# Kernel tuning notes

Measured on AMD Instinct MI355X. Metric: run time of the kernel, lower is better.

The kernel has to match this reference:

```python
import jax, jax.numpy as jnp
import numpy as np

D_MODEL = 1024
NHEAD = 16
EPS = 1e-5


def layer_norm(x, scale, bias):
    mu = jnp.mean(x, axis=-1, keepdims=True)
    var = jnp.var(x, axis=-1, keepdims=True)
    return (x - mu) * jax.lax.rsqrt(var + EPS) * scale + bias


def setup_inputs() -> dict:
    key = jax.random.key(0)
    ks = jax.random.split(key, 8)
    B, S, D = 4, 2048, D_MODEL
    s = 1.0 / np.sqrt(D)
    return {
        "x": jax.random.normal(ks[0], (B, S, D), dtype=jnp.float32),
        "Wq": jax.random.normal(ks[1], (D, D), dtype=jnp.float32) * s,
        "Wk": jax.random.normal(ks[2], (D, D), dtype=jnp.float32) * s,
        "Wv": jax.random.normal(ks[3], (D, D), dtype=jnp.float32) * s,
        "W1": jax.random.normal(ks[4], (D, D), dtype=jnp.float32) * s,
        "b1": jnp.zeros((D,), dtype=jnp.float32),
        "W2": jax.random.normal(ks[5], (D, D), dtype=jnp.float32) * s,
        "b2": jnp.zeros((D,), dtype=jnp.float32),
        "ln1_scale": jnp.ones((D,), dtype=jnp.float32),
        "ln1_bias": jnp.zeros((D,), dtype=jnp.float32),
        "ln2_scale": jnp.ones((D,), dtype=jnp.float32),
        "ln2_bias": jnp.zeros((D,), dtype=jnp.float32),
    }


def reference(x, Wq, Wk, Wv, W1, b1, W2, b2, ln1_scale, ln1_bias, ln2_scale, ln2_bias):
    B, S, D = x.shape
    H = NHEAD
    dh = D // H
    x = layer_norm(x, ln1_scale, ln1_bias)
    # torch Linear: y = x @ W.T (no bias for q/k/v)
    q = jnp.einsum('bsd,ed->bse', x, Wq).reshape(B, S, H, dh).transpose(0, 2, 1, 3)
    k = jnp.einsum('bsd,ed->bse', x, Wk).reshape(B, S, H, dh).transpose(0, 2, 1, 3)
    v = jnp.einsum('bsd,ed->bse', x, Wv).reshape(B, S, H, dh).transpose(0, 2, 1, 3)
    # NOTE: original module applies NO 1/sqrt(dh) scaling — kept faithful.
    scores = jnp.einsum('bhqd,bhkd->bhqk', q, k)
    attn = jax.nn.softmax(scores, axis=-1)  # dropout is identity in eval
    att = jnp.einsum('bhqk,bhkd->bhqd', attn, v)
    att = att.transpose(0, 2, 1, 3).reshape(B, S, D)
    xt = layer_norm(x + att, ln2_scale, ln2_bias)
    h = jax.nn.relu(jnp.einsum('bsd,ed->bse', xt, W1) + b1)
    ffn = jnp.einsum('bsd,ed->bse', h, W2) + b2
    return xt + ffn
```

## Files before the change

kernel.cpp:

```cpp
#include <hip/hip_runtime.h>
#include <stdint.h>

typedef unsigned short u16;
typedef __attribute__((ext_vector_type(4))) float f32x4;
typedef _Float16 h16;
typedef __attribute__((ext_vector_type(8))) _Float16 f16x8;
typedef __attribute__((ext_vector_type(4))) _Float16 h16x4;
typedef __attribute__((ext_vector_type(2))) __fp16 fp16v2;

#define DMODEL 1024
#define SEQ    2048
#define BATCH  4
#define NHEAD  16
#define DH     64
#define NTOK   (BATCH*SEQ)
#define BH     (BATCH*NHEAD)
#define EPS    1e-5f
#define LOG2E  1.44269504f

__device__ __forceinline__ void gload_lds16(const void* g, void* l){
  __builtin_amdgcn_global_load_lds((__attribute__((address_space(1))) unsigned int*)g,
                                   (__attribute__((address_space(3))) unsigned int*)l,
                                   16, 0, 0);
}

__device__ __forceinline__ float fastexp2(float x){
#if __has_builtin(__builtin_amdgcn_exp2f)
  return __builtin_amdgcn_exp2f(x);
#else
  return exp2f(x);
#endif
}

__device__ __forceinline__ int swzkey(int row){ return (row&7) ^ ((row>>3)&7); }

__global__ __launch_bounds__(256) void prep_weights(const float* __restrict__ Wq,
                                                    const float* __restrict__ Wk,
                                                    const float* __restrict__ Wv,
                                                    const float* __restrict__ W1,
                                                    const float* __restrict__ W2,
                                                    h16* __restrict__ wqkv,
                                                    h16* __restrict__ w1h,
                                                    h16* __restrict__ w2h){
  const int nW = DMODEL*DMODEL;
  int r = blockIdx.x >> 10;
  int i = ((blockIdx.x & 1023)*256 + threadIdx.x)*4;
  const float* src = (r==0) ? Wq : (r==1) ? Wk : (r==2) ? Wv : (r==3) ? W1 : W2;
  h16* dst = (r==0) ? wqkv : (r==1) ? (wqkv+nW) : (r==2) ? (wqkv+2*nW) : (r==3) ? w1h : w2h;
  float4 v = *reinterpret_cast<const float4*>(src + i);
  h16x4 o; o[0]=(h16)v.x; o[1]=(h16)v.y; o[2]=(h16)v.z; o[3]=(h16)v.w;
  *reinterpret_cast<h16x4*>(dst + i) = o;
}

__global__ __launch_bounds__(256) void ln_kernel(const float* __restrict__ in0,
                                                 const float* __restrict__ sc,
                                                 const float* __restrict__ bi,
                                                 float* __restrict__ of32,
                                                 h16* __restrict__ oh16){
  int row = blockIdx.x*4 + (threadIdx.x>>6);
  int l = threadIdx.x & 63;
  size_t rbase = (size_t)row*DMODEL;
  float v[16];
  #pragma unroll
  for (int q=0;q<4;++q){
    float4 t = *reinterpret_cast<const float4*>(in0 + rbase + q*256 + l*4);
    v[q*4]=t.x; v[q*4+1]=t.y; v[q*4+2]=t.z; v[q*4+3]=t.w;
  }
  float s=0.f, ss=0.f;
  #pragma unroll
  for (int j=0;j<16;++j){ s += v[j]; ss += v[j]*v[j]; }
  #pragma unroll
  for (int m=1;m<64;m<<=1){ s += __shfl_xor(s,m); ss += __shfl_xor(ss,m); }
  float mu  = s * (1.0f/DMODEL);
  float var = fmaxf(ss * (1.0f/DMODEL) - mu*mu, 0.0f);
  float r = rsqrtf(var + EPS);
  #pragma unroll
  for (int q=0;q<4;++q){
    float4 g = *reinterpret_cast<const float4*>(sc + q*256 + l*4);
    float4 b = *reinterpret_cast<const float4*>(bi + q*256 + l*4);
    float o0 = (v[q*4  ]-mu)*r*g.x + b.x;
    float o1 = (v[q*4+1]-mu)*r*g.y + b.y;
    float o2 = (v[q*4+2]-mu)*r*g.z + b.z;
    float o3 = (v[q*4+3]-mu)*r*g.w + b.w;
    size_t off = rbase + q*256 + l*4;
    if (of32){
      float4 ov; ov.x=o0; ov.y=o1; ov.z=o2; ov.w=o3;
      *reinterpret_cast<float4*>(of32 + off) = ov;
    }
    if (oh16){
      h16x4 oh; oh[0]=(h16)o0; oh[1]=(h16)o1; oh[2]=(h16)o2; oh[3]=(h16)o3;
      *reinterpret_cast<h16x4*>(oh16 + off) = oh;
    }
  }
}

__global__ __launch_bounds__(256) void gemm_qkv(const h16* __restrict__ xn,
                                                const h16* __restrict__ wqkv,
                                                h16* __restrict__ qT,
                                                h16* __restrict__ kR,
                                                h16* __restrict__ vT){
  const int K = DMODEL;
  __shared__ h16 As[128*64], Bs[128*64];
  int id = blockIdx.x;
  int xcd = id & 7, j = id >> 3;
  int bm = xcd*8 + j/24;
  int bn = j - (j/24)*24;
  int t = threadIdx.x, l = t&63, w = t>>6;
  int wr = w>>1, wc = w&1;
  const h16* Bsrc = wqkv + (size_t)bn*128*K;

  f32x4 acc[4][4];
  #pragma unroll
  for (int m=0;m<4;++m)
    #pragma unroll
    for (int n=0;n<4;++n)
      #pragma unroll
      for (int i=0;i<4;++i) acc[m][n][i] = 0.0f;

  const int nk = K/64;
  for (int kt=0; kt<nk; ++kt){
    int k0 = kt*64;
    __syncthreads();
    #pragma unroll
    for (int i=0;i<4;++i){
      int slot = i*256 + t;
      int row = slot>>3, pc = slot&7;
      int lc = pc ^ swzkey(row);
      gload_lds16(xn + (size_t)(bm*128 + row)*K + k0 + lc*8, &As[slot*8]);
      gload_lds16(Bsrc + (size_t)row*K + k0 + lc*8, &Bs[slot*8]);
    }
    __syncthreads();
    #pragma unroll
    for (int ks=0; ks<2; ++ks){
      f16x8 af[4], bf[4];
      #pragma unroll
      for (int m=0;m<4;++m){
        int row = wr*64 + m*16 + (l&15);
        int cp = (ks*4 + (l>>4)) ^ swzkey(row);
        af[m] = *reinterpret_cast<const f16x8*>(&As[row*64 + cp*8]);
      }
      #pragma unroll
      for (int n=0;n<4;++n){
        int row = wc*64 + n*16 + (l&15);
        int cp = (ks*4 + (l>>4)) ^ swzkey(row);
        bf[n] = *reinterpret_cast<const f16x8*>(&Bs[row*64 + cp*8]);
      }
      __builtin_amdgcn_s_setprio(1);
      #pragma unroll
      for (int m=0;m<4;++m)
        #pragma unroll
        for (int n=0;n<4;++n)
          acc[m][n] = __builtin_amdgcn_mfma_f32_16x16x32_f16(af[m], bf[n], acc[m][n], 0,0,0);
      __builtin_amdgcn_s_setprio(0);
    }
  }

  const bool isK = (bn >= 8 && bn < 16);
  const bool isQ = (bn < 8);
  #pragma unroll
  for (int m=0;m<4;++m){
    int row0 = bm*128 + wr*64 + m*16 + ((l>>4)<<2);
    int b = row0 >> 11, s0 = row0 & 2047;
    #pragma unroll
    for (int n=0;n<4;++n){
      int col = bn*128 + wc*64 + n*16 + (l&15);
      int dg = col & 1023;
      int hh = dg >> 6, dh = dg & 63;
      if (isK){
        #pragma unroll
        for (int i=0;i<4;++i)
          kR[((size_t)(b*NHEAD + hh)*SEQ + s0 + i)*DH + dh] = (h16)acc[m][n][i];
      } else {
        h16x4 ov;
        #pragma unroll
        for (int i=0;i<4;++i){
          float vv = acc[m][n][i];
          if (isQ) vv *= LOG2E;
          ov[i] = (h16)vv;
        }
        int s0p = isQ ? s0 : ((s0 & ~31) + (((s0>>2)&3)<<3) + (((s0>>4)&1)<<2));
        h16* dst = (isQ ? qT : vT) + ((size_t)(b*NHEAD + hh)*DH + dh)*SEQ + s0p;
        *reinterpret_cast<h16x4*>(dst) = ov;
      }
    }
  }
}

template<bool RELU, bool RES, bool OUTF32>
__global__ __launch_bounds__(256) void gemm_ffn(const h16* __restrict__ A,
                                                const h16* __restrict__ W,
                                                const float* __restrict__ bias,
                                                const float* __restrict__ resid,
                                                void* __restrict__ outp,
                                                int M, int N, int K){
  __shared__ h16 As[128*64];
  __shared__ h16 Bs[128*64];
  int id = blockIdx.x;
  int xcd = id & 7, j = id >> 3;
  int nbn = N >> 7;
  int bm = xcd*((M>>7)>>3) + j/nbn;
  int bn = j - (j/nbn)*nbn;
  int t = threadIdx.x, l = t&63, w = t>>6;
  int wr = w>>1, wc = w&1;
  f32x4 acc[4][4];
  #pragma unroll
  for (int m=0;m<4;++m)
    #pragma unroll
    for (int n=0;n<4;++n)
      #pragma unroll
      for (int i=0;i<4;++i) acc[m][n][i] = 0.0f;

  const int nk = K/64;
  for (int kt=0; kt<nk; ++kt){
    int k0 = kt*64;
    __syncthreads();
    #pragma unroll
    for (int i=0;i<4;++i){
      int slot = i*256 + t;
      int row = slot>>3, pc = slot&7;
      int lc = pc ^ swzkey(row);
      gload_lds16(A + (size_t)(bm*128 + row)*K + k0 + lc*8, &As[slot*8]);
      gload_lds16(W + (size_t)(bn*128 + row)*K + k0 + lc*8, &Bs[slot*8]);
    }
    __syncthreads();
    #pragma unroll
    for (int ks=0; ks<2; ++ks){
      f16x8 af[4], bf[4];
      #pragma unroll
      for (int m=0;m<4;++m){
        int row = wr*64 + m*16 + (l&15);
        int cp = (ks*4 + (l>>4)) ^ swzkey(row);
        af[m] = *reinterpret_cast<const f16x8*>(&As[row*64 + cp*8]);
      }
      #pragma unroll
      for (int n=0;n<4;++n){
        int row = wc*64 + n*16 + (l&15);
        int cp = (ks*4 + (l>>4)) ^ swzkey(row);
        bf[n] = *reinterpret_cast<const f16x8*>(&Bs[row*64 + cp*8]);
      }
      __builtin_amdgcn_s_setprio(1);
      #pragma unroll
      for (int m=0;m<4;++m)
        #pragma unroll
        for (int n=0;n<4;++n)
          acc[m][n] = __builtin_amdgcn_mfma_f32_16x16x32_f16(af[m], bf[n], acc[m][n], 0,0,0);
      __builtin_amdgcn_s_setprio(0);
    }
  }

  #pragma unroll
  for (int m=0;m<4;++m){
    int row0 = bm*128 + wr*64 + m*16 + ((l>>4)<<2);
    #pragma unroll
    for (int n=0;n<4;++n){
      int col = bn*128 + wc*64 + n*16 + (l&15);
      float bv = bias[col];
      #pragma unroll
      for (int i=0;i<4;++i){
        float vv = acc[m][n][i] + bv;
        if (RELU) vv = fmaxf(vv, 0.0f);
        size_t off = (size_t)(row0+i)*N + col;
        if (RES) vv += resid[off];
        if (OUTF32) ((float*)outp)[off] = vv;
        else        ((h16*)outp)[off] = (h16)vv;
      }
    }
  }
}

#define QBLK 256
#define KBLK 64
#define RESC_THR_L2 11.5415603f
#define NROWS (BH*8*256)

__global__ __launch_bounds__(512, 2) void attn_split(const h16* __restrict__ qT,
                                                     const h16* __restrict__ kR,
                                                     const h16* __restrict__ vT,
                                                     h16* __restrict__ outP0,
                                                     h16* __restrict__ outP1,
                                                     float2* __restrict__ lm){
  int id = blockIdx.x;
  int bh   = (id & 7) + ((id >> 7) << 3);
  int qb   = (id >> 3) & 7;
  int half = (id >> 6) & 1;
  int t = threadIdx.x, l = t&63, w = t>>6;
  int g = l>>4;

  const size_t hbase = (size_t)bh * SEQ * DH;
  const h16* khb = kR + hbase + (size_t)half*(SEQ/2)*DH;
  const h16* qtb = qT + hbase;
  const h16* vtb = vT + hbase + half*(SEQ/2);
  int q0 = qb*QBLK + w*32;

  f16x8 qf[2][2];
  #pragma unroll
  for (int qs=0;qs<2;++qs)
    #pragma unroll
    for (int kc=0;kc<2;++kc)
      #pragma unroll
      for (int j=0;j<8;++j)
        qf[qs][kc][j] = qtb[(size_t)(kc*32 + g*8 + j)*SEQ + q0 + qs*16 + (l&15)];

  __shared__ h16 Kh2[2][KBLK*64];
  __shared__ h16 Vt2[2][KBLK*64];

  int offs[8];
  #pragma unroll
  for (int kc=0;kc<2;++kc)
    #pragma unroll
    for (int st=0;st<4;++st){
      int rr = st*16 + (l&15);
      offs[kc*4+st] = rr*128 + (((kc*4 + g) ^ swzkey(rr))<<4);
    }

  int srow = t>>3, spc = t&7;
  int slc = spc ^ swzkey(srow);
  const h16* ksrc = khb + (size_t)srow*DH + slc*8;
  const h16* vsrc = vtb + (size_t)srow*SEQ + slc*8;

  f32x4 o[2][4];
  #pragma unroll
  for (int qs=0;qs<2;++qs)
    #pragma unroll
    for (int dt=0;dt<4;++dt)
      #pragma unroll
      for (int i=0;i<4;++i) o[qs][dt][i] = 0.0f;
  f32x4 lacc[2];
  #pragma unroll
  for (int qs=0;qs<2;++qs)
    #pragma unroll
    for (int i=0;i<4;++i) lacc[qs][i] = 0.0f;
  float m_run[2] = {-3.0e38f, -3.0e38f};

  f16x8 onesA;
  #pragma unroll
  for (int j=0;j<8;++j) onesA[j] = (h16)1.0f;

  #define STAGE(bb)                                  \
    { gload_lds16(ksrc, &Kh2[bb][t*8]);              \
      gload_lds16(vsrc, &Vt2[bb][t*8]);              \
      ksrc += KBLK*DH; vsrc += KBLK; }

  STAGE(0);
  int cur = 0;
  const int NT = SEQ/2/KBLK;
  for (int kt=0; kt<NT; ++kt){
    __syncthreads();
    if (kt+1 < NT) STAGE(cur^1);

    char* KhB = (char*)&Kh2[cur][0];
    char* VtB = (char*)&Vt2[cur][0];

    f32x4 sc[2][4];
    #pragma unroll
    for (int qs=0;qs<2;++qs)
      #pragma unroll
      for (int st=0;st<4;++st)
        #pragma unroll
        for (int i=0;i<4;++i) sc[qs][st][i] = 0.0f;

    #pragma unroll
    for (int kc=0;kc<2;++kc)
      #pragma unroll
      for (int st=0;st<4;++st){
        f16x8 kf = *reinterpret_cast<const f16x8*>(KhB + offs[kc*4+st]);
        __builtin_amdgcn_s_setprio(1);
        sc[0][st] = __builtin_amdgcn_mfma_f32_16x16x32_f16(kf, qf[0][kc], sc[0][st], 0,0,0);
        sc[1][st] = __builtin_amdgcn_mfma_f32_16x16x32_f16(kf, qf[1][kc], sc[1][st], 0,0,0);
        __builtin_amdgcn_s_setprio(0);
      }

    float lmax[2];
    #pragma unroll
    for (int qs=0;qs<2;++qs){
      const float* s = (const float*)&sc[qs][0];
      float m0 = fmaxf(s[0], s[1]);
      #pragma unroll
      for (int j=2;j<16;j+=2) m0 = fmaxf(fmaxf(m0, s[j]), s[j+1]);
      lmax[qs] = m0;
    }
    bool defer = (__all((lmax[0] <= m_run[0] + RESC_THR_L2) &&
                        (lmax[1] <= m_run[1] + RESC_THR_L2)) != 0);
    if (!defer){
      #pragma unroll
      for (int qs=0;qs<2;++qs){
        float m0 = lmax[qs];
        m0 = fmaxf(m0, __shfl_xor(m0, 16));
        m0 = fmaxf(m0, __shfl_xor(m0, 32));
        float mn = fmaxf(m_run[qs], m0);
        float scl = fastexp2(m_run[qs] - mn);
        m_run[qs] = mn;
        #pragma unroll
        for (int dt=0;dt<4;++dt)
          #pragma unroll
          for (int i=0;i<4;++i) o[qs][dt][i] *= scl;
        #pragma unroll
        for (int i=0;i<4;++i) lacc[qs][i] *= scl;
      }
    }

    union { unsigned u[4]; f16x8 v; } pfu[2][2];
    #pragma unroll
    for (int qs=0;qs<2;++qs){
      float mn = m_run[qs];
      const float* s = (const float*)&sc[qs][0];
      #pragma unroll
      for (int kc=0;kc<2;++kc)
        #pragma unroll
        for (int j=0;j<4;++j){
          float p0 = fastexp2(s[kc*8+2*j]   - mn);
          float p1 = fastexp2(s[kc*8+2*j+1] - mn);
          union { fp16v2 v2; unsigned u; } c;
          c.v2 = __builtin_amdgcn_cvt_pkrtz(p0, p1);
          pfu[qs][kc].u[j] = c.u;
        }
    }

    #pragma unroll
    for (int kc=0;kc<2;++kc){
      __builtin_amdgcn_s_setprio(1);
      lacc[0] = __builtin_amdgcn_mfma_f32_16x16x32_f16(onesA, pfu[0][kc].v, lacc[0], 0,0,0);
      lacc[1] = __builtin_amdgcn_mfma_f32_16x16x32_f16(onesA, pfu[1][kc].v, lacc[1], 0,0,0);
      __builtin_amdgcn_s_setprio(0);
      #pragma unroll
      for (int dt=0;dt<4;++dt){
        f16x8 vf = *reinterpret_cast<const f16x8*>(VtB + offs[kc*4+dt]);
        __builtin_amdgcn_s_setprio(1);
        o[0][dt] = __builtin_amdgcn_mfma_f32_16x16x32_f16(vf, pfu[0][kc].v, o[0][dt], 0,0,0);
        o[1][dt] = __builtin_amdgcn_mfma_f32_16x16x32_f16(vf, pfu[1][kc].v, o[1][dt], 0,0,0);
        __builtin_amdgcn_s_setprio(0);
      }
    }
    cur ^= 1;
  }

  h16* outP = half ? outP1 : outP0;
  int rowbase = (bh*8 + qb)*256 + w*32;
  #pragma unroll
  for (int qs=0;qs<2;++qs){
    float lt = lacc[qs][0];
    float inv = 1.0f / lt;
    int row = rowbase + qs*16 + (l&15);
    #pragma unroll
    for (int dt=0;dt<4;++dt){
      h16x4 ov;
      #pragma unroll
      for (int i=0;i<4;++i) ov[i] = (h16)(o[qs][dt][i] * inv);
      *reinterpret_cast<h16x4*>(outP + (size_t)row*64 + dt*16 + (g<<2)) = ov;
    }
    if (l < 16)
      lm[half*NROWS + row] = make_float2(m_run[qs], lt);
  }
}

__global__ __launch_bounds__(256) void ln2_combine(const float* __restrict__ xn,
                                                   const h16* __restrict__ p0,
                                                   const h16* __restrict__ p1,
                                                   const float2* __restrict__ lm,
                                                   const float* __restrict__ sc,
                                                   const float* __restrict__ bi,
                                                   float* __restrict__ of32,
                                                   h16* __restrict__ oh16){
  int token = blockIdx.x*4 + (threadIdx.x>>6);
  int l = threadIdx.x & 63;
  int b = token >> 11, qb = (token >> 8) & 7, r = token & 255;
  int hh = l >> 2;
  int rowg = ((b*NHEAD + hh)*8 + qb)*256 + r;
  float2 A = lm[rowg];
  float2 B = lm[NROWS + rowg];
  float ms = fmaxf(A.x, B.x);
  float w0 = A.y * fastexp2(A.x - ms);
  float w1 = B.y * fastexp2(B.x - ms);
  float inv = 1.0f / (w0 + w1);
  w0 *= inv; w1 *= inv;

  const f16x8* q0 = reinterpret_cast<const f16x8*>(p0 + (size_t)rowg*64 + (l&3)*16);
  const f16x8* q1 = reinterpret_cast<const f16x8*>(p1 + (size_t)rowg*64 + (l&3)*16);
  size_t base = (size_t)token*DMODEL + l*16;
  float v[16];
  #pragma unroll
  for (int c=0;c<2;++c){
    f16x8 a = q0[c], bb = q1[c];
    #pragma unroll
    for (int j=0;j<8;++j)
      v[c*8+j] = (float)a[j]*w0 + (float)bb[j]*w1;
  }
  #pragma unroll
  for (int q=0;q<4;++q){
    float4 t = *reinterpret_cast<const float4*>(xn + base + q*4);
    v[q*4] += t.x; v[q*4+1] += t.y; v[q*4+2] += t.z; v[q*4+3] += t.w;
  }

  float s=0.f, ss=0.f;
  #pragma unroll
  for (int j=0;j<16;++j){ s += v[j]; ss += v[j]*v[j]; }
  #pragma unroll
  for (int m=1;m<64;m<<=1){ s += __shfl_xor(s,m); ss += __shfl_xor(ss,m); }
  float mu  = s * (1.0f/DMODEL);
  float var = fmaxf(ss * (1.0f/DMODEL) - mu*mu, 0.0f);
  float rr = rsqrtf(var + EPS);
  #pragma unroll
  for (int q=0;q<4;++q){
    float4 g = *reinterpret_cast<const float4*>(sc + l*16 + q*4);
    float4 bb = *reinterpret_cast<const float4*>(bi + l*16 + q*4);
    float o0 = (v[q*4  ]-mu)*rr*g.x + bb.x;
    float o1 = (v[q*4+1]-mu)*rr*g.y + bb.y;
    float o2 = (v[q*4+2]-mu)*rr*g.z + bb.z;
    float o3 = (v[q*4+3]-mu)*rr*g.w + bb.w;
    float4 ov; ov.x=o0; ov.y=o1; ov.z=o2; ov.w=o3;
    *reinterpret_cast<float4*>(of32 + base + q*4) = ov;
    h16x4 oh; oh[0]=(h16)o0; oh[1]=(h16)o1; oh[2]=(h16)o2; oh[3]=(h16)o3;
    *reinterpret_cast<h16x4*>(oh16 + base + q*4) = oh;
  }
}

extern "C" void kernel_launch(void* const* d_in, const int* in_sizes, int n_in,
                              void* d_out, int out_size, void* d_ws, size_t ws_size,
                              hipStream_t stream){
  (void)in_sizes; (void)n_in; (void)out_size; (void)ws_size;
  const float* x    = (const float*)d_in[0];
  const float* Wq   = (const float*)d_in[1];
  const float* Wk   = (const float*)d_in[2];
  const float* Wv   = (const float*)d_in[3];
  const float* W1   = (const float*)d_in[4];
  const float* b1   = (const float*)d_in[5];
  const float* W2   = (const float*)d_in[6];
  const float* b2   = (const float*)d_in[7];
  const float* ln1s = (const float*)d_in[8];
  const float* ln1b = (const float*)d_in[9];
  const float* ln2s = (const float*)d_in[10];
  const float* ln2b = (const float*)d_in[11];

  char* ws = (char*)d_ws;
  float* xn_f32  = (float*)ws;  ws += (size_t)NTOK*DMODEL*4;
  h16* part0     = (h16*)ws;    ws += (size_t)NTOK*DMODEL*2;
  h16* part1     = (h16*)ws;    ws += (size_t)NTOK*DMODEL*2;
  float* xt_f32  = (float*)ws;  ws += (size_t)NTOK*DMODEL*4;
  h16* xn_h      = (h16*)ws;    ws += (size_t)NTOK*DMODEL*2;
  h16* qT_h      = (h16*)ws;    ws += (size_t)NTOK*DMODEL*2;
  h16* k_h       = (h16*)ws;    ws += (size_t)NTOK*DMODEL*2;
  h16* vT_h      = (h16*)ws;    ws += (size_t)NTOK*DMODEL*2;
  h16* xt_h      = (h16*)ws;    ws += (size_t)NTOK*DMODEL*2;
  h16* h_h       = (h16*)ws;    ws += (size_t)NTOK*DMODEL*2;
  h16* wqkv_h    = (h16*)ws;    ws += (size_t)3*DMODEL*DMODEL*2;
  h16* w1h       = (h16*)ws;    ws += (size_t)DMODEL*DMODEL*2;
  h16* w2h       = (h16*)ws;    ws += (size_t)DMODEL*DMODEL*2;
  float2* lm     = (float2*)ws; ws += (size_t)2*NROWS*8;

  prep_weights<<<5120, 256, 0, stream>>>(Wq, Wk, Wv, W1, W2, wqkv_h, w1h, w2h);

  ln_kernel<<<NTOK/4, 256, 0, stream>>>(x, ln1s, ln1b, xn_f32, xn_h);

  gemm_qkv<<<3*DMODEL/128 * (NTOK/128), 256, 0, stream>>>(
      xn_h, wqkv_h, qT_h, k_h, vT_h);

  attn_split<<<BH*(SEQ/QBLK)*2, 512, 0, stream>>>(qT_h, k_h, vT_h, part0, part1, lm);

  ln2_combine<<<NTOK/4, 256, 0, stream>>>(xn_f32, part0, part1, lm,
                                          ln2s, ln2b, xt_f32, xt_h);

  gemm_ffn<true,false,false><<<(DMODEL/128) * (NTOK/128), 256, 0, stream>>>(
      xt_h, w1h, b1, nullptr, h_h, NTOK, DMODEL, DMODEL);

  gemm_ffn<false,true,true><<<(DMODEL/128) * (NTOK/128), 256, 0, stream>>>(
      h_h, w2h, b2, xt_f32, d_out, NTOK, DMODEL, DMODEL);
}
```

Before: 273.6 us.

## Double-buffer LDS tiles in QKV and FFN GEMMs to overlap loads with MFMA

Both the QKV projection GEMM and the templated FFN GEMM now keep two LDS buffers for the A and B tiles. The next k-tile is prefetched with global_load_lds while the current tile is consumed by MFMAs, and each iteration now has one barrier instead of two. The aim is to hide global-memory latency and cut barrier stalls. In exchange, LDS per block doubles to 64 KB, which may reduce how many blocks fit on each CU.

```diff
diff --git a/kernel.cpp b/kernel.cpp
--- a/kernel.cpp
+++ b/kernel.cpp
@@ -100,7 +100,7 @@
                                                 h16* __restrict__ kR,
                                                 h16* __restrict__ vT){
   const int K = DMODEL;
-  __shared__ h16 As[128*64], Bs[128*64];
+  __shared__ h16 As[2][128*64], Bs[2][128*64];
   int id = blockIdx.x;
   int xcd = id & 7, j = id >> 3;
   int bm = xcd*8 + j/24;
@@ -117,19 +117,22 @@
       #pragma unroll
       for (int i=0;i<4;++i) acc[m][n][i] = 0.0f;
 
+  #define QSTAGE(bb, k0)                                                          \
+    { _Pragma("unroll")                                                           \
+      for (int i_=0;i_<4;++i_){                                                   \
+        int slot = i_*256 + t;                                                    \
+        int row = slot>>3, pc = slot&7;                                           \
+        int lc = pc ^ swzkey(row);                                                \
+        gload_lds16(xn + (size_t)(bm*128 + row)*K + (k0) + lc*8, &As[bb][slot*8]);\
+        gload_lds16(Bsrc + (size_t)row*K + (k0) + lc*8, &Bs[bb][slot*8]);         \
+      } }
+
   const int nk = K/64;
+  QSTAGE(0, 0);
+  int cur = 0;
   for (int kt=0; kt<nk; ++kt){
-    int k0 = kt*64;
     __syncthreads();
-    #pragma unroll
-    for (int i=0;i<4;++i){
-      int slot = i*256 + t;
-      int row = slot>>3, pc = slot&7;
-      int lc = pc ^ swzkey(row);
-      gload_lds16(xn + (size_t)(bm*128 + row)*K + k0 + lc*8, &As[slot*8]);
-      gload_lds16(Bsrc + (size_t)row*K + k0 + lc*8, &Bs[slot*8]);
-    }
-    __syncthreads();
+    if (kt+1 < nk) QSTAGE(cur^1, (kt+1)*64);
     #pragma unroll
     for (int ks=0; ks<2; ++ks){
       f16x8 af[4], bf[4];
@@ -137,13 +140,13 @@
       for (int m=0;m<4;++m){
         int row = wr*64 + m*16 + (l&15);
         int cp = (ks*4 + (l>>4)) ^ swzkey(row);
-        af[m] = *reinterpret_cast<const f16x8*>(&As[row*64 + cp*8]);
+        af[m] = *reinterpret_cast<const f16x8*>(&As[cur][row*64 + cp*8]);
       }
       #pragma unroll
       for (int n=0;n<4;++n){
         int row = wc*64 + n*16 + (l&15);
         int cp = (ks*4 + (l>>4)) ^ swzkey(row);
-        bf[n] = *reinterpret_cast<const f16x8*>(&Bs[row*64 + cp*8]);
+        bf[n] = *reinterpret_cast<const f16x8*>(&Bs[cur][row*64 + cp*8]);
       }
       __builtin_amdgcn_s_setprio(1);
       #pragma unroll
@@ -153,6 +156,7 @@
           acc[m][n] = __builtin_amdgcn_mfma_f32_16x16x32_f16(af[m], bf[n], acc[m][n], 0,0,0);
       __builtin_amdgcn_s_setprio(0);
     }
+    cur ^= 1;
   }
 
   const bool isK = (bn >= 8 && bn < 16);
@@ -193,8 +197,8 @@
                                                 const float* __restrict__ resid,
                                                 void* __restrict__ outp,
                                                 int M, int N, int K){
-  __shared__ h16 As[128*64];
-  __shared__ h16 Bs[128*64];
+  __shared__ h16 As[2][128*64];
+  __shared__ h16 Bs[2][128*64];
   int id = blockIdx.x;
   int xcd = id & 7, j = id >> 3;
   int nbn = N >> 7;
@@ -210,19 +214,22 @@
       #pragma unroll
       for (int i=0;i<4;++i) acc[m][n][i] = 0.0f;
 
+  #define FSTAGE(bb, k0)                                                          \
+    { _Pragma("unroll")                                                           \
+      for (int i_=0;i_<4;++i_){                                                   \
+        int slot = i_*256 + t;                                                    \
+        int row = slot>>3, pc = slot&7;                                           \
+        int lc = pc ^ swzkey(row);                                                \
+        gload_lds16(A + (size_t)(bm*128 + row)*K + (k0) + lc*8, &As[bb][slot*8]); \
+        gload_lds16(W + (size_t)(bn*128 + row)*K + (k0) + lc*8, &Bs[bb][slot*8]); \
+      } }
+
   const int nk = K/64;
+  FSTAGE(0, 0);
+  int cur = 0;
   for (int kt=0; kt<nk; ++kt){
-    int k0 = kt*64;
     __syncthreads();
-    #pragma unroll
-    for (int i=0;i<4;++i){
-      int slot = i*256 + t;
-      int row = slot>>3, pc = slot&7;
-      int lc = pc ^ swzkey(row);
-      gload_lds16(A + (size_t)(bm*128 + row)*K + k0 + lc*8, &As[slot*8]);
-      gload_lds16(W + (size_t)(bn*128 + row)*K + k0 + lc*8, &Bs[slot*8]);
-    }
-    __syncthreads();
+    if (kt+1 < nk) FSTAGE(cur^1, (kt+1)*64);
     #pragma unroll
     for (int ks=0; ks<2; ++ks){
       f16x8 af[4], bf[4];
@@ -230,13 +237,13 @@
       for (int m=0;m<4;++m){
         int row = wr*64 + m*16 + (l&15);
         int cp = (ks*4 + (l>>4)) ^ swzkey(row);
-        af[m] = *reinterpret_cast<const f16x8*>(&As[row*64 + cp*8]);
+        af[m] = *reinterpret_cast<const f16x8*>(&As[cur][row*64 + cp*8]);
       }
       #pragma unroll
       for (int n=0;n<4;++n){
         int row = wc*64 + n*16 + (l&15);
         int cp = (ks*4 + (l>>4)) ^ swzkey(row);
-        bf[n] = *reinterpret_cast<const f16x8*>(&Bs[row*64 + cp*8]);
+        bf[n] = *reinterpret_cast<const f16x8*>(&Bs[cur][row*64 + cp*8]);
       }
       __builtin_amdgcn_s_setprio(1);
       #pragma unroll
@@ -246,6 +253,7 @@
           acc[m][n] = __builtin_amdgcn_mfma_f32_16x16x32_f16(af[m], bf[n], acc[m][n], 0,0,0);
       __builtin_amdgcn_s_setprio(0);
     }
+    cur ^= 1;
   }
 
   #pragma unroll
```

Result: no change. 270.9 us (-1.0%).
